# Optimization experiments

Hardware: AMD Instinct MI355X
Metric: run time of the kernel (lower is better)

Reference implementation:

```python
import jax, jax.numpy as jnp
import numpy as np
from jax import lax

EPS = 1e-5
DN = ('NCHW', 'OIHW', 'NCHW')

def _sign(v):
    # (v >= 0) * 2 - 1
    return jnp.where(v >= 0, 1.0, -1.0).astype(v.dtype)

def _conv(x, w, b):
    y = lax.conv_general_dilated(x, w, (1, 1), 'VALID', dimension_numbers=DN)
    return y + b[None, :, None, None]

def _bn(x):
    # BatchNorm2d(affine=False), training mode: biased batch stats over (N,H,W)
    m = jnp.mean(x, axis=(0, 2, 3), keepdims=True)
    v = jnp.var(x, axis=(0, 2, 3), keepdims=True)
    return (x - m) * lax.rsqrt(v + EPS)

def setup_inputs() -> dict:
    key = jax.random.key(0)
    ks = jax.random.split(key, 9)
    f = jnp.float32
    B = 8192
    x = jax.random.normal(ks[0], (B, 1, 28, 28), dtype=f)
    # conv params, clipped to [-1, 1] as in clip_weights()
    w1 = jnp.clip(jax.random.normal(ks[1], (32, 1, 9, 9), dtype=f) * 0.1, -1, 1)
    b1 = jnp.clip(jax.random.normal(ks[2], (32,), dtype=f) * 0.1, -1, 1)
    w2 = jnp.clip(jax.random.normal(ks[3], (16, 32, 9, 9), dtype=f) * 0.1, -1, 1)
    b2 = jnp.clip(jax.random.normal(ks[4], (16,), dtype=f) * 0.1, -1, 1)
    w3 = jnp.clip(jax.random.normal(ks[5], (8, 16, 9, 9), dtype=f) * 0.1, -1, 1)
    b3 = jnp.clip(jax.random.normal(ks[6], (8,), dtype=f) * 0.1, -1, 1)
    wl = jnp.clip(jax.random.normal(ks[7], (10, 8, 4, 4), dtype=f) * 0.1, -1, 1)
    bl = jnp.clip(jax.random.normal(ks[8], (10,), dtype=f) * 0.1, -1, 1)
    return {"x": x, "w1": w1, "b1": b1, "w2": w2, "b2": b2,
            "w3": w3, "b3": b3, "wl": wl, "bl": bl}

def _block(x, w, b, act=True, norm=True, binarized=True):
    if binarized:
        w, b = _sign(w), _sign(b)
    x = _conv(x, w, b)
    if norm:
        x = _bn(x)
    if act:
        x = _sign(x) if binarized else jax.nn.relu(x)
    return x

def reference(x, w1, b1, w2, b2, w3, b3, wl, bl):
    x = _sign(x)                        # binarize input activations
    x = _block(x, w1, b1)               # (B, 32, 20, 20)
    x = _block(x, w2, b2)               # (B, 16, 12, 12)
    x = _block(x, w3, b3)               # (B,  8,  4,  4)
    x = _block(x, wl, bl, act=False, norm=False)  # (B, 10, 1, 1), binarized weights
    return x.reshape(-1, 10)
```

## Files before the change

### kernel.cpp

```cpp
#include <hip/hip_runtime.h>
#include <stdint.h>

#define BATCH 8192

#define OFF_W1R3   0
#define OFF_W2P    384
#define OFF_W3P    7296
#define OFF_WLB    10752
#define OFF_SBL    10912
#define OFF_TTOT   10960
#define OFF_S3     11288
#define OFF_S2PART 11360
#define OFF_Z2     76800
#define OFF_Z3     37825792


__global__ __launch_bounds__(256) void k1_pack_tsum(const float* __restrict__ x,
                                                    const float* __restrict__ w1,
                                                    const float* __restrict__ w2,
                                                    const float* __restrict__ w3,
                                                    const float* __restrict__ wl,
                                                    const float* __restrict__ bl,
                                                    uint8_t* __restrict__ ws) {
  int* Ttot = (int*)(ws + OFF_TTOT);
  const int tid = threadIdx.x;

  if (blockIdx.x == 0) {
    uint32_t* W1R3 = (uint32_t*)(ws + OFF_W1R3);
    uint32_t* W2P  = (uint32_t*)(ws + OFF_W2P);
    uint32_t* W3P  = (uint32_t*)(ws + OFF_W3P);
    uint64_t* WLB  = (uint64_t*)(ws + OFF_WLB);
    float*    SBL  = (float*)(ws + OFF_SBL);
    for (int e = tid; e < 96; e += 256) {
      int oc = e / 3, i = e % 3;
      uint32_t m = 0;
      for (int rr = 0; rr < 3; ++rr)
        for (int kw = 0; kw < 9; ++kw)
          if (w1[oc*81 + (3*i+rr)*9 + kw] < 0.f) m |= 1u << (rr*9 + kw);
      W1R3[e] = m;
    }
    for (int e = tid; e < 1296; e += 256) {
      int oc = e / 81, k = e % 81;
      int kh = k / 9, kw = k % 9;
      uint32_t m = 0;
      for (int ic = 0; ic < 32; ++ic)
        if (w2[(oc*32 + ic)*81 + k] < 0.f) m |= 1u << ic;
      W2P[(oc*9 + kh)*12 + kw] = m;
    }
    for (int e = tid; e < 432; e += 256) {
      int row = e / 3, p = e % 3;
      W2P[row*12 + 9 + p] = 0;
    }
    for (int e = tid; e < 648; e += 256) {
      int oc = e / 81, k = e % 81;
      int kh = k / 9, kw = k % 9;
      uint32_t m = 0;
      for (int ic = 0; ic < 16; ++ic)
        if (w3[(oc*16 + ic)*81 + k] < 0.f) m |= 1u << ic;
      W3P[(oc*9 + kh)*12 + kw] = m;
    }
    for (int e = tid; e < 216; e += 256) {
      int row = e / 3, p = e % 3;
      W3P[row*12 + 9 + p] = 0;
    }
    for (int e = tid; e < 20; e += 256) {
      int oc = e >> 1, word = e & 1;
      uint64_t m = 0;
      for (int b = 0; b < 64; ++b)
        if (wl[oc*128 + word*64 + b] < 0.f) m |= 1ull << b;
      WLB[e] = m;
    }
    if (tid < 10) SBL[tid] = (bl[tid] >= 0.f) ? 1.f : -1.f;
  }

  __shared__ uint32_t rowm[896];
  __shared__ int Tacc[81];
  if (tid < 81) Tacc[tid] = 0;
  __syncthreads();

  const int img0 = blockIdx.x * 32;
  #pragma unroll
  for (int it = 0; it < 4; ++it) {
    int R = tid + it*256;
    if (R < 896) {
      int il = R / 28, r = R % 28;
      const float4* xr = (const float4*)(x + (size_t)(img0 + il) * 784 + r * 28);
      uint32_t m = 0;
      #pragma unroll
      for (int j = 0; j < 7; ++j) {
        float4 v = xr[j];
        if (v.x < 0.f) m |= 1u << (j*4+0);
        if (v.y < 0.f) m |= 1u << (j*4+1);
        if (v.z < 0.f) m |= 1u << (j*4+2);
        if (v.w < 0.f) m |= 1u << (j*4+3);
      }
      rowm[R] = m;
    }
  }
  __syncthreads();

  for (int T = tid; T < 288; T += 256) {
    int il = T / 9, kw = T % 9;
    int base = il * 28;
    int n9[9];
    int sum20 = 0;
    #pragma unroll
    for (int r = 0; r < 20; ++r) {
      int n = __popc((rowm[base + r] >> kw) & 0xFFFFFu);
      if (r < 9) n9[r] = n;
      sum20 += n;
    }
    atomicAdd(&Tacc[kw], 400 - 2*sum20);
    #pragma unroll
    for (int kh = 1; kh <= 8; ++kh) {
      int nadd = __popc((rowm[base + kh + 19] >> kw) & 0xFFFFFu);
      sum20 += nadd - n9[kh-1];
      atomicAdd(&Tacc[kh*9 + kw], 400 - 2*sum20);
    }
  }
  __syncthreads();
  if (tid < 81) atomicAdd(&Ttot[tid], Tacc[tid]);
}

#define K2_IMGS 4
__global__ __launch_bounds__(256) void k2_conv12(const float* __restrict__ x,
                                                 uint8_t* __restrict__ ws) {
  const uint32_t* W1R3g = (const uint32_t*)(ws + OFF_W1R3);
  const uint32_t* W2Pg  = (const uint32_t*)(ws + OFF_W2P);
  const int* Ttot = (const int*)(ws + OFF_TTOT);
  int* S2P = (int*)(ws + OFF_S2PART);

  __shared__ uint32_t __attribute__((aligned(16))) rowm[K2_IMGS*28];
  __shared__ uint32_t __attribute__((aligned(16))) w1r3[96];
  __shared__ uint32_t __attribute__((aligned(16))) w2p[1728];
  __shared__ int tlds[81];
  __shared__ int t1s[32];
  __shared__ uint32_t __attribute__((aligned(16))) A1s[K2_IMGS*400];
  __shared__ int s2acc[16];

  const int tid = threadIdx.x;
  const int img0 = blockIdx.x * K2_IMGS;

  for (int e = tid; e < 96; e += 256)   w1r3[e] = W1R3g[e];
  for (int e = tid; e < 1728; e += 256) w2p[e]  = W2Pg[e];
  if (tid < 81) tlds[tid] = Ttot[tid];
  if (tid < 16) s2acc[tid] = 0;
  if (tid < K2_IMGS*28) {
    int il = tid / 28, rr = tid % 28;
    const float4* xr = (const float4*)(x + (size_t)(img0 + il) * 784 + rr * 28);
    uint32_t m = 0;
    #pragma unroll
    for (int j = 0; j < 7; ++j) {
      float4 v = xr[j];
      if (v.x < 0.f) m |= 1u << (j*4+0);
      if (v.y < 0.f) m |= 1u << (j*4+1);
      if (v.z < 0.f) m |= 1u << (j*4+2);
      if (v.w < 0.f) m |= 1u << (j*4+3);
    }
    rowm[tid] = m;
  }
  __syncthreads();

  if (tid < 32) {
    long long S = 0;
    for (int kh = 0; kh < 9; ++kh)
      for (int kw = 0; kw < 9; ++kw) {
        int bit = (w1r3[tid*3 + kh/3] >> ((kh%3)*9 + kw)) & 1;
        S += (long long)(1 - 2*bit) * tlds[kh*9 + kw];
      }
    const long long N1 = (long long)BATCH * 400;
    long long q = S / N1, rr = S % N1;
    long long t = q + (rr > 0 ? 1 : 0);
    if ((t & 1) == 0) t += 1;
    t1s[tid] = (int)((81 - t) / 2);
  }
  __syncthreads();

  for (int G = tid; G < K2_IMGS*80; G += 256) {
    int il = G / 80, rem = G - il*80;
    int oh = rem >> 2, ow0 = (rem & 3) * 5;
    uint32_t R[9];
    #pragma unroll
    for (int i = 0; i < 9; ++i) R[i] = rowm[il*28 + oh + i];
    uint32_t win[5][3];
    #pragma unroll
    for (int j = 0; j < 5; ++j) {
      int ow = ow0 + j;
      #pragma unroll
      for (int i = 0; i < 3; ++i) {
        uint32_t b0 = (R[3*i]   >> ow) & 0x1FFu;
        uint32_t b1 = (R[3*i+1] >> ow) & 0x1FFu;
        uint32_t b2 = (R[3*i+2] >> ow) & 0x1FFu;
        win[j][i] = b0 | (b1 << 9) | (b2 << 18);
      }
    }
    uint32_t mask[5] = {0,0,0,0,0};
    #pragma unroll
    for (int ocg = 0; ocg < 4; ++ocg) {
      const uint4* wp = (const uint4*)&w1r3[ocg*24];
      uint32_t wr[24];
      #pragma unroll
      for (int q = 0; q < 6; ++q) {
        uint4 v = wp[q];
        wr[q*4+0]=v.x; wr[q*4+1]=v.y; wr[q*4+2]=v.z; wr[q*4+3]=v.w;
      }
      #pragma unroll
      for (int o8 = 0; o8 < 8; ++o8) {
        int oc = ocg*8 + o8;
        int thr = t1s[oc];
        #pragma unroll
        for (int j = 0; j < 5; ++j) {
          int mm = __popc(win[j][0] ^ wr[o8*3])
                 + __popc(win[j][1] ^ wr[o8*3+1])
                 + __popc(win[j][2] ^ wr[o8*3+2]);
          mask[j] |= (uint32_t)(mm > thr) << oc;
        }
      }
    }
    #pragma unroll
    for (int j = 0; j < 5; ++j) A1s[il*400 + oh*20 + ow0 + j] = mask[j];
  }
  __syncthreads();

  uint32_t* Z2w = (uint32_t*)(ws + OFF_Z2);
  const int oc = tid & 15;
  const int par = oc & 1;
  const uint32_t* W = &w2p[oc*108];
  int sl = 0;
  for (int r = 0; r < 3; ++r) {
    const int G = tid + r*256;
    const int grp = G >> 4;
    const int il = grp / 12, oy = grp - il*12;
    const uint32_t* A = &A1s[il*400 + oy*20];
    int acc[12];
    #pragma unroll
    for (int p = 0; p < 12; ++p) acc[p] = 0;
    #pragma unroll 1
    for (int kh = 0; kh < 9; ++kh) {
      const uint4* ar = (const uint4*)(A + kh*20);
      uint4 v0 = ar[0], v1 = ar[1], v2 = ar[2], v3 = ar[3], v4 = ar[4];
      uint32_t a[20] = {v0.x,v0.y,v0.z,v0.w, v1.x,v1.y,v1.z,v1.w,
                        v2.x,v2.y,v2.z,v2.w, v3.x,v3.y,v3.z,v3.w,
                        v4.x,v4.y,v4.z,v4.w};
      const uint4* wr4 = (const uint4*)(W + kh*12);
      uint4 w0 = wr4[0], w1v = wr4[1], w2v = wr4[2];
      uint32_t w[9] = {w0.x,w0.y,w0.z,w0.w, w1v.x,w1v.y,w1v.z,w1v.w, w2v.x};
      #pragma unroll
      for (int kw = 0; kw < 9; ++kw) {
        #pragma unroll
        for (int px = 0; px < 12; ++px)
          acc[px] += __popc(a[kw+px] ^ w[kw]);
      }
    }
    int z[12];
    int s = 0;
    #pragma unroll
    for (int px = 0; px < 12; ++px) { z[px] = 2592 - 2*acc[px]; s += z[px]; }
    sl += s;
    size_t base = (size_t)(img0+il)*1152 + (size_t)oy*96 + (oc >> 1);
    #pragma unroll
    for (int j = 0; j < 6; ++j) {
      int send = par ? z[j] : z[6+j];
      int recv = __shfl_xor(send, 1);
      uint32_t val = par
        ? ((uint32_t)(uint16_t)(int16_t)recv   | ((uint32_t)(uint16_t)(int16_t)z[6+j] << 16))
        : ((uint32_t)(uint16_t)(int16_t)z[j]   | ((uint32_t)(uint16_t)(int16_t)recv   << 16));
      int px = par ? (6+j) : j;
      Z2w[base + (size_t)px*8] = val;
    }
  }
  atomicAdd(&s2acc[oc], sl);
  __syncthreads();
  if (tid < 16) atomicAdd(&S2P[(blockIdx.x & 255)*16 + tid], s2acc[tid]);
}

__global__ __launch_bounds__(256) void k3_conv3(uint8_t* __restrict__ ws) {
  const int* S2P = (const int*)(ws + OFF_S2PART);
  const uint32_t* W3Pg = (const uint32_t*)(ws + OFF_W3P);
  const uint32_t* Z2w = (const uint32_t*)(ws + OFF_Z2);
  uint32_t* Z3w = (uint32_t*)(ws + OFF_Z3);
  unsigned long long* S3 = (unsigned long long*)(ws + OFF_S3);

  __shared__ uint32_t __attribute__((aligned(16))) w3p[864];
  __shared__ int part[256];
  __shared__ int t2s[16];
  __shared__ uint32_t __attribute__((aligned(16))) A2[32*144];
  __shared__ int s3acc[8];

  const int tid = threadIdx.x;
  const int img0 = blockIdx.x * 32;

  {
    int c = tid & 15, g = tid >> 4;
    int s = 0;
    for (int j = 0; j < 16; ++j) s += S2P[(g + 16*j)*16 + c];
    part[tid] = s;
  }
  for (int e = tid; e < 864; e += 256) w3p[e] = W3Pg[e];
  if (tid < 8) s3acc[tid] = 0;
  __syncthreads();
  if (tid < 16) {
    long long S = 0;
    #pragma unroll
    for (int g = 0; g < 16; ++g) S += (long long)part[g*16 + tid];
    const long long N2 = (long long)BATCH * 144;
    long long q = S / N2, r = S % N2;
    long long t = q + (r > 0 ? 1 : 0);
    if (t & 1) t += 1;
    t2s[tid] = (int)t;
  }
  __syncthreads();

  #pragma unroll
  for (int j = 0; j < 18; ++j) {
    int idx = tid + j*256;
    const uint4* zp = (const uint4*)&Z2w[(size_t)(img0 + idx/144)*1152 + (size_t)(idx%144)*8];
    uint4 v0 = zp[0], v1 = zp[1];
    uint32_t zz[8] = {v0.x,v0.y,v0.z,v0.w, v1.x,v1.y,v1.z,v1.w};
    uint32_t m = 0;
    #pragma unroll
    for (int i = 0; i < 8; ++i) {
      int zlo = (int)(short)(zz[i] & 0xFFFFu);
      int zhi = (int)zz[i] >> 16;
      m |= (uint32_t)(zlo < t2s[2*i])   << (2*i);
      m |= (uint32_t)(zhi < t2s[2*i+1]) << (2*i+1);
    }
    A2[idx] = m;
  }
  __syncthreads();

  const int il = tid >> 3, oc = tid & 7;
  int acc[16];
  #pragma unroll
  for (int i = 0; i < 16; ++i) acc[i] = 0;
  #pragma unroll
  for (int r = 0; r < 12; ++r) {
    const uint4* ar = (const uint4*)&A2[il*144 + r*12];
    uint4 v0 = ar[0], v1 = ar[1], v2 = ar[2];
    uint32_t a[12] = {v0.x,v0.y,v0.z,v0.w, v1.x,v1.y,v1.z,v1.w, v2.x,v2.y,v2.z,v2.w};
    #pragma unroll
    for (int oy = 0; oy < 4; ++oy) {
      if (r - oy >= 0 && r - oy <= 8) {
        int kh = r - oy;
        const uint4* wr = (const uint4*)&w3p[(oc*9 + kh)*12];
        uint4 w0 = wr[0], w1v = wr[1], w2v = wr[2];
        uint32_t w[9] = {w0.x,w0.y,w0.z,w0.w, w1v.x,w1v.y,w1v.z,w1v.w, w2v.x};
        #pragma unroll
        for (int ox = 0; ox < 4; ++ox) {
          int m = 0;
          #pragma unroll
          for (int kw = 0; kw < 9; ++kw) m += __popc(a[ox+kw] ^ w[kw]);
          acc[oy*4+ox] += m;
        }
      }
    }
  }
  int ssum = 0;
  uint32_t packed[8];
  #pragma unroll
  for (int h = 0; h < 8; ++h) {
    int za = 1296 - 2*acc[2*h], zb = 1296 - 2*acc[2*h+1];
    ssum += za + zb;
    packed[h] = (uint32_t)(uint16_t)(int16_t)za | ((uint32_t)(uint16_t)(int16_t)zb << 16);
  }
  uint4* zp = (uint4*)&Z3w[(size_t)(img0 + il)*64 + oc*8];
  zp[0] = make_uint4(packed[0], packed[1], packed[2], packed[3]);
  zp[1] = make_uint4(packed[4], packed[5], packed[6], packed[7]);
  atomicAdd(&s3acc[oc], ssum);
  __syncthreads();
  if (tid < 8)
    atomicAdd(&S3[tid], (unsigned long long)(long long)s3acc[tid]);
}

__global__ __launch_bounds__(64) void k4_final(uint8_t* __restrict__ ws,
                                               float* __restrict__ out) {
  const uint32_t* Z3w = (const uint32_t*)(ws + OFF_Z3);
  const long long* S3 = (const long long*)(ws + OFF_S3);
  const uint64_t* WLBg = (const uint64_t*)(ws + OFF_WLB);
  const float* SBLg = (const float*)(ws + OFF_SBL);
  __shared__ int t3[8];
  __shared__ uint64_t wlb[20];
  __shared__ float sbl[10];
  const int tid = threadIdx.x;
  if (tid < 8) {
    long long S = S3[tid];
    const long long N3 = (long long)BATCH * 16;
    long long q = S / N3, r = S % N3;
    long long t = q + (r > 0 ? 1 : 0);
    if (t & 1) t += 1;
    t3[tid] = (int)t;
  }
  if (tid < 20) wlb[tid] = WLBg[tid];
  if (tid < 10) sbl[tid] = SBLg[tid];
  __syncthreads();
  int img = blockIdx.x * 64 + tid;
  const uint4* zp = (const uint4*)&Z3w[(size_t)img * 64];
  uint32_t zz[64];
  #pragma unroll
  for (int q = 0; q < 16; ++q) {
    uint4 v = zp[q];
    zz[q*4+0]=v.x; zz[q*4+1]=v.y; zz[q*4+2]=v.z; zz[q*4+3]=v.w;
  }
  uint64_t a0 = 0, a1 = 0;
  #pragma unroll
  for (int j = 0; j < 64; ++j) {
    int z = (j & 1) ? ((int)zz[j>>1] >> 16) : (int)(short)(zz[j>>1] & 0xFFFFu);
    a0 |= (uint64_t)(z < t3[j >> 4]) << j;
  }
  #pragma unroll
  for (int j = 0; j < 64; ++j) {
    int z = (j & 1) ? ((int)zz[32 + (j>>1)] >> 16) : (int)(short)(zz[32 + (j>>1)] & 0xFFFFu);
    a1 |= (uint64_t)(z < t3[(64 + j) >> 4]) << j;
  }
  #pragma unroll
  for (int oc = 0; oc < 10; ++oc) {
    int mism = __popcll(a0 ^ wlb[oc*2]) + __popcll(a1 ^ wlb[oc*2 + 1]);
    out[(size_t)img*10 + oc] = (float)(128 - 2*mism) + sbl[oc];
  }
}

extern "C" void kernel_launch(void* const* d_in, const int* in_sizes, int n_in,
                              void* d_out, int out_size, void* d_ws, size_t ws_size,
                              hipStream_t stream) {
  (void)in_sizes; (void)n_in; (void)out_size; (void)ws_size;
  const float* x  = (const float*)d_in[0];
  const float* w1 = (const float*)d_in[1];
  const float* w2 = (const float*)d_in[3];
  const float* w3 = (const float*)d_in[5];
  const float* wl = (const float*)d_in[7];
  const float* bl = (const float*)d_in[8];
  uint8_t* ws = (uint8_t*)d_ws;
  float* out = (float*)d_out;

  hipMemsetAsync(ws + OFF_TTOT, 0, OFF_S2PART + 256*16*4 - OFF_TTOT, stream);
  k1_pack_tsum<<<256, 256, 0, stream>>>(x, w1, w2, w3, wl, bl, ws);
  k2_conv12<<<2048, 256, 0, stream>>>(x, ws);
  k3_conv3<<<256, 256, 0, stream>>>(ws);
  k4_final<<<128, 64, 0, stream>>>(ws, out);
}
```

Baseline: 260.9 us.

## Compute conv2 with int8 MFMA on ±1 bytes instead of XOR-popcount

Conv2 weights are repacked as ±1 int8 bytes, and layer-1 sign bitmasks are expanded to ±1 int8 per channel in shared memory. The inner loop becomes __builtin_amdgcn_mfma_i32_16x16x64_i8 over 81 taps × 2 channel halves instead of per-thread XOR+popcount accumulation. Images per block drop from 4 to 2 and the grid doubles so the larger LDS footprint fits. The aim is to move the dominant conv2 arithmetic onto matrix cores. The cost is 8x larger activation storage in LDS, a bigger weight copy per block and a more complex output shuffle.

```diff
diff --git a/kernel.cpp b/kernel.cpp
--- a/kernel.cpp
+++ b/kernel.cpp
@@ -4,16 +4,18 @@
 #define BATCH 8192
 
 #define OFF_W1R3   0
-#define OFF_W2P    384
 #define OFF_W3P    7296
 #define OFF_WLB    10752
 #define OFF_SBL    10912
 #define OFF_TTOT   10960
 #define OFF_S3     11288
 #define OFF_S2PART 11360
+#define OFF_W2I8   28672
 #define OFF_Z2     76800
 #define OFF_Z3     37825792
 
+
+typedef int v4i __attribute__((ext_vector_type(4)));
 
 __global__ __launch_bounds__(256) void k1_pack_tsum(const float* __restrict__ x,
                                                     const float* __restrict__ w1,
@@ -27,10 +29,10 @@
 
   if (blockIdx.x == 0) {
     uint32_t* W1R3 = (uint32_t*)(ws + OFF_W1R3);
-    uint32_t* W2P  = (uint32_t*)(ws + OFF_W2P);
     uint32_t* W3P  = (uint32_t*)(ws + OFF_W3P);
     uint64_t* WLB  = (uint64_t*)(ws + OFF_WLB);
     float*    SBL  = (float*)(ws + OFF_SBL);
+    uint32_t* W2I8d = (uint32_t*)(ws + OFF_W2I8);
     for (int e = tid; e < 96; e += 256) {
       int oc = e / 3, i = e % 3;
       uint32_t m = 0;
@@ -39,17 +41,20 @@
           if (w1[oc*81 + (3*i+rr)*9 + kw] < 0.f) m |= 1u << (rr*9 + kw);
       W1R3[e] = m;
     }
-    for (int e = tid; e < 1296; e += 256) {
-      int oc = e / 81, k = e % 81;
-      int kh = k / 9, kw = k % 9;
-      uint32_t m = 0;
-      for (int ic = 0; ic < 32; ++ic)
-        if (w2[(oc*32 + ic)*81 + k] < 0.f) m |= 1u << ic;
-      W2P[(oc*9 + kh)*12 + kw] = m;
-    }
-    for (int e = tid; e < 432; e += 256) {
-      int row = e / 3, p = e % 3;
-      W2P[row*12 + 9 + p] = 0;
+    for (int e = tid; e < 10496; e += 256) {
+      int c = e >> 6;
+      int rem = e & 63;
+      int oc = rem >> 2, j0 = (rem & 3) * 4;
+      int tap = c >> 1, h = c & 1;
+      uint32_t d = 0;
+      if (tap < 81) {
+        for (int b = 0; b < 4; ++b) {
+          int ic = h*16 + j0 + b;
+          uint32_t by = (w2[(oc*32 + ic)*81 + tap] < 0.f) ? 0xFFu : 0x01u;
+          d |= by << (8*b);
+        }
+      }
+      W2I8d[e] = d;
     }
     for (int e = tid; e < 648; e += 256) {
       int oc = e / 81, k = e % 81;
@@ -122,27 +127,30 @@
   if (tid < 81) atomicAdd(&Ttot[tid], Tacc[tid]);
 }
 
-#define K2_IMGS 4
+#define K2_IMGS 2
 __global__ __launch_bounds__(256) void k2_conv12(const float* __restrict__ x,
                                                  uint8_t* __restrict__ ws) {
   const uint32_t* W1R3g = (const uint32_t*)(ws + OFF_W1R3);
-  const uint32_t* W2Pg  = (const uint32_t*)(ws + OFF_W2P);
   const int* Ttot = (const int*)(ws + OFF_TTOT);
   int* S2P = (int*)(ws + OFF_S2PART);
 
-  __shared__ uint32_t __attribute__((aligned(16))) rowm[K2_IMGS*28];
+  __shared__ uint32_t rowm[K2_IMGS*28];
   __shared__ uint32_t __attribute__((aligned(16))) w1r3[96];
-  __shared__ uint32_t __attribute__((aligned(16))) w2p[1728];
   __shared__ int tlds[81];
   __shared__ int t1s[32];
-  __shared__ uint32_t __attribute__((aligned(16))) A1s[K2_IMGS*400];
   __shared__ int s2acc[16];
+  __shared__ uint32_t __attribute__((aligned(16))) A1d[K2_IMGS*3200];
+  __shared__ uint32_t __attribute__((aligned(16))) w2b[10496];
 
   const int tid = threadIdx.x;
   const int img0 = blockIdx.x * K2_IMGS;
 
-  for (int e = tid; e < 96; e += 256)   w1r3[e] = W1R3g[e];
-  for (int e = tid; e < 1728; e += 256) w2p[e]  = W2Pg[e];
+  for (int e = tid; e < 96; e += 256) w1r3[e] = W1R3g[e];
+  {
+    const uint4* src = (const uint4*)(ws + OFF_W2I8);
+    uint4* dst = (uint4*)w2b;
+    for (int e = tid; e < 2624; e += 256) dst[e] = src[e];
+  }
   if (tid < 81) tlds[tid] = Ttot[tid];
   if (tid < 16) s2acc[tid] = 0;
   if (tid < K2_IMGS*28) {
@@ -218,58 +226,86 @@
       }
     }
     #pragma unroll
-    for (int j = 0; j < 5; ++j) A1s[il*400 + oh*20 + ow0 + j] = mask[j];
-  }
-  __syncthreads();
-
-  uint32_t* Z2w = (uint32_t*)(ws + OFF_Z2);
-  const int oc = tid & 15;
-  const int par = oc & 1;
-  const uint32_t* W = &w2p[oc*108];
-  int sl = 0;
-  for (int r = 0; r < 3; ++r) {
-    const int G = tid + r*256;
-    const int grp = G >> 4;
-    const int il = grp / 12, oy = grp - il*12;
-    const uint32_t* A = &A1s[il*400 + oy*20];
-    int acc[12];
-    #pragma unroll
-    for (int p = 0; p < 12; ++p) acc[p] = 0;
+    for (int j = 0; j < 5; ++j) {
+      uint32_t m32 = mask[j];
+      int px20 = oh*20 + ow0 + j;
+      uint32_t dw[8];
+      #pragma unroll
+      for (int q = 0; q < 8; ++q) {
+        uint32_t nib = (m32 >> (4*q)) & 15u;
+        uint32_t y = (nib * 0x00204081u) & 0x01010101u;
+        dw[q] = 0x01010101u ^ (y * 0xFEu);
+      }
+      uint4* dst = (uint4*)&A1d[il*3200 + px20*8];
+      dst[0] = make_uint4(dw[0],dw[1],dw[2],dw[3]);
+      dst[1] = make_uint4(dw[4],dw[5],dw[6],dw[7]);
+    }
+  }
+  __syncthreads();
+
+  {
+    const int lane = tid & 63;
+    const int wv = tid >> 6;
+    const int il = wv >> 1, half = wv & 1;
+    const int g = lane >> 4, oc = lane & 15;
+    const int NT = 5 - half;
+    int pxq[5];
+    #pragma unroll
+    for (int tt = 0; tt < 5; ++tt) {
+      int tg = half*5 + tt;
+      int px = tg*16 + oc;
+      int oh2 = (px * 171) >> 11;
+      int ow2 = px - oh2*12;
+      pxq[tt] = oh2*20 + ow2;
+    }
+    v4i acc[5];
+    #pragma unroll
+    for (int tt = 0; tt < 5; ++tt) acc[tt] = (v4i){0,0,0,0};
+    const int abase = il*3200;
     #pragma unroll 1
-    for (int kh = 0; kh < 9; ++kh) {
-      const uint4* ar = (const uint4*)(A + kh*20);
-      uint4 v0 = ar[0], v1 = ar[1], v2 = ar[2], v3 = ar[3], v4 = ar[4];
-      uint32_t a[20] = {v0.x,v0.y,v0.z,v0.w, v1.x,v1.y,v1.z,v1.w,
-                        v2.x,v2.y,v2.z,v2.w, v3.x,v3.y,v3.z,v3.w,
-                        v4.x,v4.y,v4.z,v4.w};
-      const uint4* wr4 = (const uint4*)(W + kh*12);
-      uint4 w0 = wr4[0], w1v = wr4[1], w2v = wr4[2];
-      uint32_t w[9] = {w0.x,w0.y,w0.z,w0.w, w1v.x,w1v.y,w1v.z,w1v.w, w2v.x};
-      #pragma unroll
-      for (int kw = 0; kw < 9; ++kw) {
+    for (int m = 0; m < 41; ++m) {
+      int c = 4*m + g;
+      int tap = c >> 1; tap = tap > 80 ? 80 : tap;
+      int h = c & 1;
+      int kh = (tap * 57) >> 9;
+      int toff = tap + 11*kh;
+      v4i bv = *(const v4i*)&w2b[c*64 + oc*4];
+      #pragma unroll
+      for (int tt = 0; tt < 5; ++tt) {
+        if (tt < NT) {
+          v4i av = *(const v4i*)&A1d[abase + (pxq[tt] + toff)*8 + h*4];
+          acc[tt] = __builtin_amdgcn_mfma_i32_16x16x64_i8(av, bv, acc[tt], 0, 0, 0);
+        }
+      }
+    }
+    uint32_t* Z2w = (uint32_t*)(ws + OFF_Z2);
+    const int par = oc & 1;
+    int sl = 0;
+    #pragma unroll
+    for (int tt = 0; tt < 5; ++tt) {
+      if (tt < NT) {
+        int tg = half*5 + tt;
+        size_t base = (size_t)(img0+il)*1152 + (size_t)(tg*16 + g*4)*8 + (oc >> 1);
         #pragma unroll
-        for (int px = 0; px < 12; ++px)
-          acc[px] += __popc(a[kw+px] ^ w[kw]);
-      }
-    }
-    int z[12];
-    int s = 0;
-    #pragma unroll
-    for (int px = 0; px < 12; ++px) { z[px] = 2592 - 2*acc[px]; s += z[px]; }
-    sl += s;
-    size_t base = (size_t)(img0+il)*1152 + (size_t)oy*96 + (oc >> 1);
-    #pragma unroll
-    for (int j = 0; j < 6; ++j) {
-      int send = par ? z[j] : z[6+j];
-      int recv = __shfl_xor(send, 1);
-      uint32_t val = par
-        ? ((uint32_t)(uint16_t)(int16_t)recv   | ((uint32_t)(uint16_t)(int16_t)z[6+j] << 16))
-        : ((uint32_t)(uint16_t)(int16_t)z[j]   | ((uint32_t)(uint16_t)(int16_t)recv   << 16));
-      int px = par ? (6+j) : j;
-      Z2w[base + (size_t)px*8] = val;
-    }
-  }
-  atomicAdd(&s2acc[oc], sl);
+        for (int r = 0; r < 4; ++r) {
+          int z = acc[tt][r];
+          sl += z;
+          int zs = __shfl_xor(z, 1);
+          if (par == 0 && r < 2) {
+            uint32_t val = ((uint32_t)(uint16_t)(int16_t)z)
+                         | ((uint32_t)(uint16_t)(int16_t)zs << 16);
+            Z2w[base + (size_t)r*8] = val;
+          }
+          if (par == 1 && r >= 2) {
+            uint32_t val = ((uint32_t)(uint16_t)(int16_t)zs)
+                         | ((uint32_t)(uint16_t)(int16_t)z << 16);
+            Z2w[base + (size_t)r*8] = val;
+          }
+        }
+      }
+    }
+    atomicAdd(&s2acc[oc], sl);
+  }
   __syncthreads();
   if (tid < 16) atomicAdd(&S2P[(blockIdx.x & 255)*16 + tid], s2acc[tid]);
 }
@@ -434,7 +470,7 @@
 
   hipMemsetAsync(ws + OFF_TTOT, 0, OFF_S2PART + 256*16*4 - OFF_TTOT, stream);
   k1_pack_tsum<<<256, 256, 0, stream>>>(x, w1, w2, w3, wl, bl, ws);
-  k2_conv12<<<2048, 256, 0, stream>>>(x, ws);
+  k2_conv12<<<4096, 256, 0, stream>>>(x, ws);
   k3_conv3<<<256, 256, 0, stream>>>(ws);
   k4_final<<<128, 64, 0, stream>>>(ws, out);
 }
```

Result: slower. 290.9 us (+11.5%).
